# Kernel optimization log

Hardware: AMD Instinct MI355X
Metric: run time of the kernel (lower is better)

Reference implementation:

```python
import jax, jax.numpy as jnp
import numpy as np

IN_C, OUT_C = 32, 64
KSIZE = (3, 3, 3)


def setup_inputs() -> dict:
    key = jax.random.key(0)
    k1, k2 = jax.random.split(key)
    x = jax.random.normal(k1, (2, IN_C, 64, 64, 64), dtype=jnp.float32)
    # One learnable scalar per (out_channel, in_channel, kz, ky, kx) basis function.
    W = jax.random.normal(k2, (OUT_C, IN_C) + KSIZE, dtype=jnp.float32) * 0.05
    return {"x": x, "W": W}


def reference(x, W):
    # Original: for each (oc, ic, kz, ky, kx), out[:, oc] += basis(x[:, ic, shifted_slices])
    # With scalar-weight bases this is exactly a VALID (unpadded) 3D convolution:
    # out[b, o, d, h, w] = sum_{i, kz, ky, kx} W[o, i, kz, ky, kx] * x[b, i, d+kz, h+ky, w+kx]
    return jax.lax.conv_general_dilated(
        x, W,
        window_strides=(1, 1, 1),
        padding="VALID",
        dimension_numbers=("NCDHW", "OIDHW", "NCDHW"),
    )
```

## Files before the change

kernel.cpp:

```cpp
#include <hip/hip_runtime.h>
#include <hip/hip_bf16.h>

#define DIN 64
#define DOUT 62
#define ICH 32
#define OCH 64

typedef __bf16 bf16x8 __attribute__((ext_vector_type(8)));
typedef float f32x4 __attribute__((ext_vector_type(4)));
typedef float f32x8 __attribute__((ext_vector_type(8)));
typedef float f32x16 __attribute__((ext_vector_type(16)));

#define AS1U(p) ((const __attribute__((address_space(1))) unsigned int*)(p))
#define AS3U(p) ((__attribute__((address_space(3))) unsigned int*)(p))

__global__ void prep_all(const float* __restrict__ x, const float* __restrict__ W,
                         unsigned short* __restrict__ Wre3, unsigned short* __restrict__ xp) {
    const int bid = blockIdx.x;
    if (bid < 8192) {
        int idx = bid * 256 + threadIdx.x;
        int w = idx & 63;
        int s = (idx >> 6) & 3;
        int y = (idx >> 8) & 63;
        int z = (idx >> 14) & 63;
        int b = idx >> 20;
        const float* xb = x + ((size_t)(b * ICH + s * 8)) * 262144 + (size_t)z * 4096 + y * 64 + w;
        bf16x8 pk;
#pragma unroll
        for (int j = 0; j < 8; ++j)
            pk[j] = (__bf16)xb[(size_t)j * 262144];
        ((int4*)xp)[idx] = __builtin_bit_cast(int4, pk);
    } else {
        int idx = (bid - 8192) * 256 + threadIdx.x;
        if (idx < 27 * OCH * ICH) {
            int j    = idx & 7;
            int lane = (idx >> 3) & 63;
            int kh   = (idx >> 9) & 1;
            int mt   = (idx >> 10) & 1;
            int tap  = idx >> 11;
            int oc   = mt * 32 + (lane & 31);
            int ic   = kh * 16 + (lane >> 5) * 8 + j;
            float v  = W[((size_t)oc * ICH + ic) * 27 + tap];
            Wre3[idx] = __builtin_bit_cast(unsigned short, (__bf16)v);
        }
    }
}

__global__ __launch_bounds__(256, 3) void conv3d_mfma_pk(
    const unsigned short* __restrict__ Wre3,
    const unsigned short* __restrict__ xp,
    float* __restrict__ out)
{
    __shared__ char xs[2 * 24576 + 256];

    const int tid  = threadIdx.x;
    const int lane = tid & 63;
    const int wave = tid >> 6;

    const int orig = blockIdx.x;
    const int lid  = (orig & 7) * 248 + (orig >> 3);
    const int ht = lid & 15;
    const int rr = lid >> 4;
    const int d  = rr % DOUT;
    const int b  = rr / DOUT;
    const int h0 = ht * 4;

    const int l31 = lane & 31;
    const int lhi = lane >> 5;
    const int row = wave;

    auto stage_chunk = [&](char* buf, int z, int i) {
        int c  = wave * 6 + i;
        int yl = c >> 2;
        int sl = c & 3;
        int srow = h0 + yl; if (srow > 63) srow = 63;
        const unsigned short* src =
            xp + ((((size_t)(b * DIN + z) * DIN + srow) * 4 + sl) * 64) * 8 + lane * 8;
        __builtin_amdgcn_global_load_lds(AS1U(src), AS3U(buf + c * 1024), 16, 0, 0);
    };
    auto loadA = [&](int tap, int4* af) {
        const int4* wp = (const int4*)Wre3 + (size_t)tap * 256 + lane;
#pragma unroll
        for (int q = 0; q < 4; ++q)
            af[q] = wp[q * 64];
    };
    auto readB = [&](const char* buf, int ky, int kx, int4* dst) {
#pragma unroll
        for (int kh = 0; kh < 2; ++kh) {
            const int g = kh * 2 + lhi;
#pragma unroll
            for (int nt = 0; nt < 2; ++nt) {
                int wb = nt * 32 + l31 + kx;
                if (wb > 63) wb = 63;
                dst[kh * 2 + nt] = *(const int4*)(buf + (((row + ky) * 4 + g) * 64 + wb) * 16);
            }
        }
    };

    char* bufA = xs;
    char* bufB = xs + 24576;

#pragma unroll
    for (int i = 0; i < 6; ++i) stage_chunk(bufA, d, i);
    int4 af[3][4];
    loadA(0, af[0]);
    loadA(1, af[1]);

    f32x16 acc[2][2];
#pragma unroll
    for (int mt = 0; mt < 2; ++mt)
#pragma unroll
        for (int nt = 0; nt < 2; ++nt)
#pragma unroll
            for (int r = 0; r < 16; ++r) acc[mt][nt][r] = 0.f;

    __syncthreads();

    int4 bfr[2][4];
    const bool oddw = (wave & 1) != 0;

#pragma unroll
    for (int kz = 0; kz < 3; ++kz) {
        char* cur = (kz & 1) ? bufB : bufA;
        char* nxt = (kz & 1) ? bufA : bufB;
        readB(cur, 0, 0, bfr[0]);

#pragma unroll
        for (int t = 0; t < 9; ++t) {
            const int T = kz * 9 + t;
            if (oddw) {
                if (t < 8)  readB(cur, (t + 1) / 3, (t + 1) % 3, bfr[(t + 1) & 1]);
                if (T < 25) loadA(T + 2, af[(T + 2) % 3]);
            } else {
                if (T < 25) loadA(T + 2, af[(T + 2) % 3]);
                if (t < 8)  readB(cur, (t + 1) / 3, (t + 1) % 3, bfr[(t + 1) & 1]);
            }
            if (kz < 2 && t < 6) stage_chunk(nxt, d + kz + 1, t);

#pragma unroll
            for (int kh = 0; kh < 2; ++kh)
#pragma unroll
                for (int mt = 0; mt < 2; ++mt)
#pragma unroll
                    for (int nt = 0; nt < 2; ++nt)
                        acc[mt][nt] = __builtin_amdgcn_mfma_f32_32x32x16_bf16(
                            __builtin_bit_cast(bf16x8, af[T % 3][mt * 2 + kh]),
                            __builtin_bit_cast(bf16x8, bfr[t & 1][kh * 2 + nt]),
                            acc[mt][nt], 0, 0, 0);
        }
        if (kz < 2) __syncthreads();
    }

    const int h = h0 + row;
    if (h < DOUT) {
#pragma unroll
        for (int mt = 0; mt < 2; ++mt) {
#pragma unroll
            for (int r = 0; r < 16; ++r) {
                int oc = mt * 32 + (r & 3) + 8 * (r >> 2) + 4 * lhi;
                size_t ob = ((((size_t)b * OCH + oc) * DOUT + d) * DOUT + h) * DOUT;
#pragma unroll
                for (int nt = 0; nt < 2; ++nt) {
                    int ww = nt * 32 + l31;
                    if (ww < DOUT) out[ob + ww] = acc[mt][nt][r];
                }
            }
        }
    }
}

__global__ __launch_bounds__(256, 3) void conv3d_mfma_fb(
    const float* __restrict__ x, const float* __restrict__ W,
    float* __restrict__ out)
{
    __shared__ char xs[2][6 * 66 * 64];

    const int tid  = threadIdx.x;
    const int lane = tid & 63;
    const int wave = tid >> 6;

    const int orig = blockIdx.x;
    const int lid  = (orig & 7) * 248 + (orig >> 3);
    const int ht = lid & 15;
    const int rr = lid >> 4;
    const int d  = rr % DOUT;
    const int b  = rr / DOUT;
    const int h0 = ht * 4;

    const int wlo = lane & 15;
    const int whi = lane >> 4;
    const int row = wave;

    const int icg  = wave;
    const int w    = lane;
    const int slot = icg ^ ((w >> 1) & 3);

    auto issueRow = [&](int z, int y) -> f32x8 {
        int gy = h0 + y; if (gy > 63) gy = 63;
        const float* xp2 = x + (((size_t)(b * ICH + icg * 8) * DIN + z) * DIN + gy) * DIN + w;
        f32x8 s;
#pragma unroll
        for (int j = 0; j < 8; ++j) s[j] = xp2[(size_t)j * DIN * DIN * DIN];
        return s;
    };
    auto writeRow = [&](char* buf, int y, f32x8 s) {
        bf16x8 pk;
#pragma unroll
        for (int j = 0; j < 8; ++j) pk[j] = (__bf16)s[j];
        *(int4*)(buf + ((y * 66 + w) * 64 + slot * 16)) = __builtin_bit_cast(int4, pk);
    };
    auto loadA = [&](int tap, int4* af) {
#pragma unroll
        for (int mt = 0; mt < 4; ++mt) {
            const float* wp = W + ((size_t)(mt * 16 + wlo) * ICH + whi * 8) * 27 + tap;
            bf16x8 t;
#pragma unroll
            for (int j = 0; j < 8; ++j) t[j] = (__bf16)wp[j * 27];
            af[mt] = __builtin_bit_cast(int4, t);
        }
    };
    auto readB = [&](const char* buf, int ky, int kx, int4* dst) {
#pragma unroll
        for (int nt = 0; nt < 4; ++nt) {
            int wb = nt * 16 + wlo + kx;
            int sl = whi ^ ((wb >> 1) & 3);
            dst[nt] = *(const int4*)(buf + (((row + ky) * 66 + wb) * 64 + sl * 16));
        }
    };

    if (tid < 96) {
        int bu = tid / 48, q2 = tid % 48;
        int y = q2 >> 3, q = q2 & 7;
        int w2 = 64 + (q >> 2), sl = q & 3;
        *(int4*)(xs[bu] + ((y * 66 + w2) * 64 + sl * 16)) = int4{0, 0, 0, 0};
    }
    {
        f32x8 s0 = issueRow(d, 0), s1 = issueRow(d, 1), s2 = issueRow(d, 2);
        writeRow(xs[0], 0, s0); s0 = issueRow(d, 3);
        writeRow(xs[0], 1, s1); s1 = issueRow(d, 4);
        writeRow(xs[0], 2, s2); s2 = issueRow(d, 5);
        writeRow(xs[0], 3, s0); writeRow(xs[0], 4, s1); writeRow(xs[0], 5, s2);
    }
    int4 af[2][4];
    loadA(0, af[0]);
    __syncthreads();

    f32x4 acc[4][4];
#pragma unroll
    for (int mt = 0; mt < 4; ++mt)
#pragma unroll
        for (int nt = 0; nt < 4; ++nt)
            acc[mt][nt] = f32x4{0.f, 0.f, 0.f, 0.f};

    int4 bfr[2][4];

#pragma unroll
    for (int kz = 0; kz < 3; ++kz) {
        char* cur = xs[kz & 1];
        char* nxt = xs[(kz + 1) & 1];
        f32x8 s0, s1, s2;
        readB(cur, 0, 0, bfr[0]);
#pragma unroll
        for (int t = 0; t < 9; ++t) {
            const int T = kz * 9 + t;
            if (T < 26) loadA(T + 1, af[(T + 1) & 1]);
            if (t < 8)  readB(cur, (t + 1) / 3, (t + 1) % 3, bfr[(t + 1) & 1]);
            if (kz < 2) {
                if (t == 3) writeRow(nxt, 0, s0);
                if (t == 4) writeRow(nxt, 1, s1);
                if (t == 5) writeRow(nxt, 2, s2);
                if (t == 6) writeRow(nxt, 3, s0);
                if (t == 7) writeRow(nxt, 4, s1);
                if (t == 8) writeRow(nxt, 5, s2);
                if (t == 0) s0 = issueRow(d + kz + 1, 0);
                if (t == 1) s1 = issueRow(d + kz + 1, 1);
                if (t == 2) s2 = issueRow(d + kz + 1, 2);
                if (t == 3) s0 = issueRow(d + kz + 1, 3);
                if (t == 4) s1 = issueRow(d + kz + 1, 4);
                if (t == 5) s2 = issueRow(d + kz + 1, 5);
            }
#pragma unroll
            for (int mt = 0; mt < 4; ++mt)
#pragma unroll
                for (int nt = 0; nt < 4; ++nt)
                    acc[mt][nt] = __builtin_amdgcn_mfma_f32_16x16x32_bf16(
                        __builtin_bit_cast(bf16x8, af[T & 1][mt]),
                        __builtin_bit_cast(bf16x8, bfr[t & 1][nt]),
                        acc[mt][nt], 0, 0, 0);
        }
        if (kz < 2) __syncthreads();
    }

    const int h = h0 + row;
    if (h < DOUT) {
#pragma unroll
        for (int mt = 0; mt < 4; ++mt) {
#pragma unroll
            for (int r = 0; r < 4; ++r) {
                int oc = mt * 16 + whi * 4 + r;
                size_t ob = ((((size_t)b * OCH + oc) * DOUT + d) * DOUT + h) * DOUT;
#pragma unroll
                for (int nt = 0; nt < 4; ++nt) {
                    int ww = nt * 16 + wlo;
                    if (ww < DOUT) out[ob + ww] = acc[mt][nt][r];
                }
            }
        }
    }
}

extern "C" void kernel_launch(void* const* d_in, const int* in_sizes, int n_in,
                              void* d_out, int out_size, void* d_ws, size_t ws_size,
                              hipStream_t stream) {
    const float* x = (const float*)d_in[0];
    const float* W = (const float*)d_in[1];
    float* out = (float*)d_out;

    const size_t wre_elems = (size_t)27 * OCH * ICH;
    const size_t xp_elems  = (size_t)2 * DIN * DIN * DIN * ICH;
    const size_t need = (wre_elems + xp_elems) * 2 + 256;

    if (ws_size >= need) {
        unsigned short* Wre3 = (unsigned short*)d_ws;
        unsigned short* xp   = Wre3 + wre_elems;
        prep_all<<<dim3(8192 + 216), 256, 0, stream>>>(x, W, Wre3, xp);
        conv3d_mfma_pk<<<dim3(2 * DOUT * 16), 256, 0, stream>>>(Wre3, xp, out);
    } else {
        conv3d_mfma_fb<<<dim3(2 * DOUT * 16), 256, 0, stream>>>(x, W, out);
    }
}
```

Measured before the change: 84.47 us.

## Split output channels across two wave groups with 512-thread blocks

Doubles the block to 8 waves, with each wave computing one output row for half of the output channels (32 instead of 64). This halves per-wave accumulators and A-fragment registers, and the staging work is spread across twice as many waves. The aim is higher occupancy and more latency hiding. In exchange, each B fragment is now read from LDS by two waves, and the launch bounds target 4 blocks of 512 threads per CU.

```diff
diff --git a/kernel.cpp b/kernel.cpp
--- a/kernel.cpp
+++ b/kernel.cpp
@@ -46,7 +46,7 @@
     }
 }
 
-__global__ __launch_bounds__(256, 3) void conv3d_mfma_pk(
+__global__ __launch_bounds__(512, 4) void conv3d_mfma_pk(
     const unsigned short* __restrict__ Wre3,
     const unsigned short* __restrict__ xp,
     float* __restrict__ out)
@@ -56,6 +56,8 @@
     const int tid  = threadIdx.x;
     const int lane = tid & 63;
     const int wave = tid >> 6;
+    const int rloc  = wave & 3;
+    const int ohalf = wave >> 2;
 
     const int orig = blockIdx.x;
     const int lid  = (orig & 7) * 248 + (orig >> 3);
@@ -67,10 +69,9 @@
 
     const int l31 = lane & 31;
     const int lhi = lane >> 5;
-    const int row = wave;
 
     auto stage_chunk = [&](char* buf, int z, int i) {
-        int c  = wave * 6 + i;
+        int c  = wave * 3 + i;
         int yl = c >> 2;
         int sl = c & 3;
         int srow = h0 + yl; if (srow > 63) srow = 63;
@@ -79,10 +80,10 @@
         __builtin_amdgcn_global_load_lds(AS1U(src), AS3U(buf + c * 1024), 16, 0, 0);
     };
     auto loadA = [&](int tap, int4* af) {
-        const int4* wp = (const int4*)Wre3 + (size_t)tap * 256 + lane;
-#pragma unroll
-        for (int q = 0; q < 4; ++q)
-            af[q] = wp[q * 64];
+        const int4* wp = (const int4*)Wre3 + (size_t)tap * 256 + ohalf * 128 + lane;
+#pragma unroll
+        for (int kh = 0; kh < 2; ++kh)
+            af[kh] = wp[kh * 64];
     };
     auto readB = [&](const char* buf, int ky, int kx, int4* dst) {
 #pragma unroll
@@ -92,7 +93,7 @@
             for (int nt = 0; nt < 2; ++nt) {
                 int wb = nt * 32 + l31 + kx;
                 if (wb > 63) wb = 63;
-                dst[kh * 2 + nt] = *(const int4*)(buf + (((row + ky) * 4 + g) * 64 + wb) * 16);
+                dst[kh * 2 + nt] = *(const int4*)(buf + (((rloc + ky) * 4 + g) * 64 + wb) * 16);
             }
         }
     };
@@ -101,18 +102,16 @@
     char* bufB = xs + 24576;
 
 #pragma unroll
-    for (int i = 0; i < 6; ++i) stage_chunk(bufA, d, i);
-    int4 af[3][4];
+    for (int i = 0; i < 3; ++i) stage_chunk(bufA, d, i);
+    int4 af[3][2];
     loadA(0, af[0]);
     loadA(1, af[1]);
 
-    f32x16 acc[2][2];
-#pragma unroll
-    for (int mt = 0; mt < 2; ++mt)
-#pragma unroll
-        for (int nt = 0; nt < 2; ++nt)
-#pragma unroll
-            for (int r = 0; r < 16; ++r) acc[mt][nt][r] = 0.f;
+    f32x16 acc[2];
+#pragma unroll
+    for (int nt = 0; nt < 2; ++nt)
+#pragma unroll
+        for (int r = 0; r < 16; ++r) acc[nt][r] = 0.f;
 
     __syncthreads();
 
@@ -135,35 +134,30 @@
                 if (T < 25) loadA(T + 2, af[(T + 2) % 3]);
                 if (t < 8)  readB(cur, (t + 1) / 3, (t + 1) % 3, bfr[(t + 1) & 1]);
             }
-            if (kz < 2 && t < 6) stage_chunk(nxt, d + kz + 1, t);
+            if (kz < 2 && t < 3) stage_chunk(nxt, d + kz + 1, t);
 
 #pragma unroll
             for (int kh = 0; kh < 2; ++kh)
 #pragma unroll
-                for (int mt = 0; mt < 2; ++mt)
-#pragma unroll
-                    for (int nt = 0; nt < 2; ++nt)
-                        acc[mt][nt] = __builtin_amdgcn_mfma_f32_32x32x16_bf16(
-                            __builtin_bit_cast(bf16x8, af[T % 3][mt * 2 + kh]),
-                            __builtin_bit_cast(bf16x8, bfr[t & 1][kh * 2 + nt]),
-                            acc[mt][nt], 0, 0, 0);
+                for (int nt = 0; nt < 2; ++nt)
+                    acc[nt] = __builtin_amdgcn_mfma_f32_32x32x16_bf16(
+                        __builtin_bit_cast(bf16x8, af[T % 3][kh]),
+                        __builtin_bit_cast(bf16x8, bfr[t & 1][kh * 2 + nt]),
+                        acc[nt], 0, 0, 0);
         }
         if (kz < 2) __syncthreads();
     }
 
-    const int h = h0 + row;
+    const int h = h0 + rloc;
     if (h < DOUT) {
 #pragma unroll
-        for (int mt = 0; mt < 2; ++mt) {
-#pragma unroll
-            for (int r = 0; r < 16; ++r) {
-                int oc = mt * 32 + (r & 3) + 8 * (r >> 2) + 4 * lhi;
-                size_t ob = ((((size_t)b * OCH + oc) * DOUT + d) * DOUT + h) * DOUT;
-#pragma unroll
-                for (int nt = 0; nt < 2; ++nt) {
-                    int ww = nt * 32 + l31;
-                    if (ww < DOUT) out[ob + ww] = acc[mt][nt][r];
-                }
+        for (int r = 0; r < 16; ++r) {
+            int oc = ohalf * 32 + (r & 3) + 8 * (r >> 2) + 4 * lhi;
+            size_t ob = ((((size_t)b * OCH + oc) * DOUT + d) * DOUT + h) * DOUT;
+#pragma unroll
+            for (int nt = 0; nt < 2; ++nt) {
+                int ww = nt * 32 + l31;
+                if (ww < DOUT) out[ob + ww] = acc[nt][r];
             }
         }
     }
@@ -324,7 +318,7 @@
         unsigned short* Wre3 = (unsigned short*)d_ws;
         unsigned short* xp   = Wre3 + wre_elems;
         prep_all<<<dim3(8192 + 216), 256, 0, stream>>>(x, W, Wre3, xp);
-        conv3d_mfma_pk<<<dim3(2 * DOUT * 16), 256, 0, stream>>>(Wre3, xp, out);
+        conv3d_mfma_pk<<<dim3(2 * DOUT * 16), 512, 0, stream>>>(Wre3, xp, out);
     } else {
         conv3d_mfma_fb<<<dim3(2 * DOUT * 16), 256, 0, stream>>>(x, W, out);
     }
```

After: 88.80 us. 5.1% more time.
